# Kernel optimization log

Hardware: AMD Instinct MI355X
Metric: run time of the kernel (lower is better)

The kernel has to match this reference:

```python
import jax, jax.numpy as jnp
import numpy as np

EPS = 1e-12  # torch F.normalize clamp

N, C, H, W = 32, 128, 128, 128
K = 64  # num_clusters


def setup_inputs() -> dict:
    key = jax.random.key(0)
    k1, k2, k3 = jax.random.split(key, 3)
    x = jax.random.normal(k1, (N, C, H, W), dtype=jnp.float32)
    conv_w = jax.random.normal(k2, (K, C), dtype=jnp.float32) * 0.1  # 1x1 conv weight, no bias
    centroids = jax.random.uniform(k3, (K, C), dtype=jnp.float32)   # torch.rand init
    return {"x": x, "conv_w": conv_w, "centroids": centroids}


def reference(x, conv_w, centroids):
    n, c = x.shape[:2]
    xf = x.reshape(n, c, -1)                       # [N, C, S], S = H*W
    # 1x1 conv == per-location matmul over channels
    soft_assign = jnp.einsum('kc,ncs->nks', conv_w, xf)
    soft_assign = jax.nn.softmax(soft_assign, axis=1)   # softmax over clusters
    # vlad[n,k,c] = sum_s a[n,k,s] * (x[n,c,s] - centroid[k,c])
    #            = (a @ x^T) - (sum_s a) * centroid   (avoids per-cluster residual tensors)
    vlad = jnp.einsum('nks,ncs->nkc', soft_assign, xf) \
           - soft_assign.sum(axis=-1)[..., None] * centroids[None, :, :]
    # intra-normalization over descriptor dim
    vlad = vlad / jnp.maximum(jnp.linalg.norm(vlad, axis=2, keepdims=True), EPS)
    flat = vlad.reshape(n, -1)                     # [N, K*C]
    flat = flat / jnp.maximum(jnp.linalg.norm(flat, axis=1, keepdims=True), EPS)
    return flat
```

## Files before the change

kernel.cpp:

```cpp
#include <hip/hip_runtime.h>
#include <hip/hip_bf16.h>

#define N_ 32
#define C_ 128
#define K_ 64
#define S_ 16384
#define TS 32
#define NCHUNK 32
#define CHUNK (S_/NCHUNK)
#define NITER (CHUNK/TS)
#define CP 136
#define LP 68
#define SP 40
#define EPS 1e-12f

typedef __attribute__((ext_vector_type(8))) short short8;
typedef __attribute__((ext_vector_type(4))) float floatx4;

__device__ inline unsigned short bfraw(float v) {
  return __builtin_bit_cast(unsigned short, __float2bfloat16(v));
}
__device__ inline float bff(unsigned short u) {
  union { unsigned int i; float f; } c; c.i = ((unsigned int)u) << 16; return c.f;
}

template <bool SLAB>
__global__ __launch_bounds__(256, 4) void vlad_main(
    const float* __restrict__ x, const float* __restrict__ w,
    float* __restrict__ vlad_out, float* __restrict__ asum_out) {
  __shared__ unsigned short sXTh[TS * CP];
  __shared__ unsigned short sXTl[TS * CP];
  __shared__ float sLog[TS * LP];
  __shared__ unsigned short sPh[K_ * SP];

  const int tid = threadIdx.x;
  const int lane = tid & 63;
  const int wv = tid >> 6;
  const int n = blockIdx.x >> 5;
  const int chunk = blockIdx.x & 31;
  const int sbase = chunk * CHUNK;

  const int lm = lane & 15;
  const int lq = lane >> 4;
  const int kb = lq * 8;

  short8 Wh[4], Wl[4];
  {
    const float* wp = w + (wv * 16 + lm) * C_;
#pragma unroll
    for (int ks = 0; ks < 4; ++ks) {
      const float* p = wp + ks * 32 + kb;
      float4 a = *(const float4*)p;
      float4 b = *(const float4*)(p + 4);
      float e[8] = {a.x, a.y, a.z, a.w, b.x, b.y, b.z, b.w};
#pragma unroll
      for (int j = 0; j < 8; ++j) {
        unsigned short h = bfraw(e[j]);
        Wh[ks][j] = (short)h;
        Wl[ks][j] = (short)bfraw(e[j] - bff(h));
      }
    }
  }

  floatx4 acc[2][4];
#pragma unroll
  for (int i = 0; i < 2; ++i)
#pragma unroll
    for (int j = 0; j < 4; ++j) acc[i][j] = (floatx4){0.f, 0.f, 0.f, 0.f};
  float accA[8];
#pragma unroll
  for (int i = 0; i < 8; ++i) accA[i] = 0.f;

  const int cA = tid & 127, hA = tid >> 7;
  const float* xstg = x + ((size_t)n * C_ + cA) * S_ + sbase + hA * 16;
  const int sC = tid >> 3, octC = tid & 7;

  float4 p0 = *(const float4*)(xstg + 0);
  float4 p1 = *(const float4*)(xstg + 4);
  float4 p2 = *(const float4*)(xstg + 8);
  float4 p3 = *(const float4*)(xstg + 12);

  for (int t = 0; t < NITER; ++t) {
    const int s0 = sbase + t * TS;

    {
      float vv[16] = {p0.x,p0.y,p0.z,p0.w, p1.x,p1.y,p1.z,p1.w,
                      p2.x,p2.y,p2.z,p2.w, p3.x,p3.y,p3.z,p3.w};
      const int sb = hA * 16;
#pragma unroll
      for (int u = 0; u < 16; ++u) {
        unsigned short h = bfraw(vv[u]);
        sXTh[(sb + u) * CP + cA] = h;
        sXTl[(sb + u) * CP + cA] = bfraw(vv[u] - bff(h));
      }
    }
    if (t + 1 < NITER) {
      const float* p = xstg + (t + 1) * TS;
      p0 = *(const float4*)(p + 0);
      p1 = *(const float4*)(p + 4);
      p2 = *(const float4*)(p + 8);
      p3 = *(const float4*)(p + 12);
    }
    __syncthreads();

#pragma unroll
    for (int st = 0; st < 2; ++st) {
      floatx4 D = {0.f, 0.f, 0.f, 0.f};
      const int srow = st * 16 + lm;
#pragma unroll
      for (int ks = 0; ks < 4; ++ks) {
        short8 Ah = *(const short8*)&sXTh[srow * CP + ks * 32 + kb];
        short8 Al = *(const short8*)&sXTl[srow * CP + ks * 32 + kb];
        D = __builtin_amdgcn_mfma_f32_16x16x32_bf16(Ah, Wh[ks], D, 0, 0, 0);
        D = __builtin_amdgcn_mfma_f32_16x16x32_bf16(Al, Wh[ks], D, 0, 0, 0);
        D = __builtin_amdgcn_mfma_f32_16x16x32_bf16(Ah, Wl[ks], D, 0, 0, 0);
      }
      const int sD = st * 16 + lq * 4;
      const int kcD = wv * 16 + lm;
#pragma unroll
      for (int r = 0; r < 4; ++r) sLog[(sD + r) * LP + kcD] = D[r];
    }
    __syncthreads();

    short8 Ah2[2], Al2[2];
    {
      float4 xa[2], xb[2];
#pragma unroll
      for (int ci = 0; ci < 2; ++ci) {
        const int crow = (wv * 2 + ci) * 16 + lm;
        const float* xp = x + ((size_t)n * C_ + crow) * S_ + s0 + kb;
        xa[ci] = *(const float4*)xp;
        xb[ci] = *(const float4*)(xp + 4);
      }

      float e[8];
      float m = -1e30f;
#pragma unroll
      for (int i = 0; i < 8; ++i) {
        e[i] = sLog[sC * LP + octC + 8 * i];
        m = fmaxf(m, e[i]);
      }
      m = fmaxf(m, __shfl_xor(m, 1));
      m = fmaxf(m, __shfl_xor(m, 2));
      m = fmaxf(m, __shfl_xor(m, 4));
      float sum = 0.f;
#pragma unroll
      for (int i = 0; i < 8; ++i) { e[i] = __expf(e[i] - m); sum += e[i]; }
      sum += __shfl_xor(sum, 1);
      sum += __shfl_xor(sum, 2);
      sum += __shfl_xor(sum, 4);
      float inv = 1.f / sum;
#pragma unroll
      for (int i = 0; i < 8; ++i) {
        float pr = e[i] * inv;
        accA[i] += pr;
        sPh[(octC + 8 * i) * SP + sC] = bfraw(pr);
      }

#pragma unroll
      for (int ci = 0; ci < 2; ++ci) {
        float ee[8] = {xa[ci].x, xa[ci].y, xa[ci].z, xa[ci].w,
                       xb[ci].x, xb[ci].y, xb[ci].z, xb[ci].w};
#pragma unroll
        for (int j = 0; j < 8; ++j) {
          unsigned short h = bfraw(ee[j]);
          Ah2[ci][j] = (short)h;
          Al2[ci][j] = (short)bfraw(ee[j] - bff(h));
        }
      }
    }
    __syncthreads();

    {
      short8 Bh[4];
#pragma unroll
      for (int kt = 0; kt < 4; ++kt)
        Bh[kt] = *(const short8*)&sPh[(kt * 16 + lm) * SP + kb];
#pragma unroll
      for (int ci = 0; ci < 2; ++ci) {
#pragma unroll
        for (int kt = 0; kt < 4; ++kt) {
          acc[ci][kt] = __builtin_amdgcn_mfma_f32_16x16x32_bf16(Ah2[ci], Bh[kt], acc[ci][kt], 0, 0, 0);
          acc[ci][kt] = __builtin_amdgcn_mfma_f32_16x16x32_bf16(Al2[ci], Bh[kt], acc[ci][kt], 0, 0, 0);
        }
      }
    }
    __syncthreads();
  }

  float* vb = vlad_out + (SLAB ? (size_t)blockIdx.x : (size_t)n) * (K_ * C_);
#pragma unroll
  for (int ci = 0; ci < 2; ++ci) {
    const int c0 = (wv * 2 + ci) * 16 + lq * 4;
#pragma unroll
    for (int kt = 0; kt < 4; ++kt) {
      const int kc = kt * 16 + lm;
      if (SLAB) {
        *(floatx4*)(vb + kc * C_ + c0) = acc[ci][kt];
      } else {
#pragma unroll
        for (int r = 0; r < 4; ++r)
          atomicAdd(vb + kc * C_ + c0 + r, acc[ci][kt][r]);
      }
    }
  }

#pragma unroll
  for (int i = 0; i < 8; ++i) sLog[tid * 8 + i] = accA[i];
  __syncthreads();
  if (tid < K_) {
    float tsum = 0.f;
    for (int s8 = 0; s8 < 32; ++s8)
      tsum += sLog[(s8 * 8 + (tid & 7)) * 8 + (tid >> 3)];
    if (SLAB) asum_out[(size_t)blockIdx.x * K_ + tid] = tsum;
    else atomicAdd(asum_out + n * K_ + tid, tsum);
  }
}

template <bool SLAB>
__global__ __launch_bounds__(128) void vlad_intra(
    const float* __restrict__ vlad_in, const float* __restrict__ asum_in,
    const float* __restrict__ cent, float* __restrict__ vlad_norm,
    float* __restrict__ gnorm) {
  const int bid = blockIdx.x;
  const int n = bid >> 6, k = bid & 63;
  const int c = threadIdx.x;

  float v, a;
  if (SLAB) {
    v = 0.f; a = 0.f;
#pragma unroll 4
    for (int ch = 0; ch < NCHUNK; ++ch) {
      v += vlad_in[((size_t)(n * NCHUNK + ch) * K_ + k) * C_ + c];
      a += asum_in[(n * NCHUNK + ch) * K_ + k];
    }
  } else {
    v = vlad_in[((size_t)(n * K_ + k)) * C_ + c];
    a = asum_in[n * K_ + k];
  }
  v -= a * cent[k * C_ + c];

  float ss = v * v;
  ss += __shfl_xor(ss, 1);  ss += __shfl_xor(ss, 2);  ss += __shfl_xor(ss, 4);
  ss += __shfl_xor(ss, 8);  ss += __shfl_xor(ss, 16); ss += __shfl_xor(ss, 32);
  __shared__ float red[2];
  if ((threadIdx.x & 63) == 0) red[threadIdx.x >> 6] = ss;
  __syncthreads();
  float total = red[0] + red[1];
  float nrm = fmaxf(sqrtf(total), EPS);
  vlad_norm[((size_t)(n * K_ + k)) * C_ + c] = v / nrm;
  if (threadIdx.x == 0) atomicAdd(gnorm + n, total / (nrm * nrm));
}

__global__ __launch_bounds__(256) void vlad_final(
    const float* __restrict__ vlad_norm, const float* __restrict__ gnorm,
    float* __restrict__ out) {
  const int idx = blockIdx.x * 256 + threadIdx.x;
  if (idx >= N_ * K_ * C_) return;
  float g = gnorm[idx >> 13];
  out[idx] = vlad_norm[idx] / fmaxf(sqrtf(g), EPS);
}

extern "C" void kernel_launch(void* const* d_in, const int* in_sizes, int n_in,
                              void* d_out, int out_size, void* d_ws, size_t ws_size,
                              hipStream_t stream) {
  const float* x    = (const float*)d_in[0];
  const float* w    = (const float*)d_in[1];
  const float* cent = (const float*)d_in[2];
  float* out = (float*)d_out;

  const int nblk = N_ * NCHUNK;
  const size_t slab_f  = (size_t)nblk * K_ * C_;
  const size_t asum_f  = (size_t)nblk * K_;
  const size_t norm_f  = (size_t)N_ * K_ * C_;
  const size_t need = (slab_f + asum_f + norm_f + N_) * sizeof(float);

  if (ws_size >= need) {
    float* slab   = (float*)d_ws;
    float* asums  = slab + slab_f;
    float* vnorm  = asums + asum_f;
    float* gnorm  = vnorm + norm_f;
    hipMemsetAsync(gnorm, 0, N_ * sizeof(float), stream);
    vlad_main<true><<<dim3(nblk), dim3(256), 0, stream>>>(x, w, slab, asums);
    vlad_intra<true><<<dim3(N_ * K_), dim3(128), 0, stream>>>(slab, asums, cent, vnorm, gnorm);
    vlad_final<<<dim3((N_ * K_ * C_ + 255) / 256), dim3(256), 0, stream>>>(vnorm, gnorm, out);
  } else {
    float* vlad_acc = (float*)d_ws;
    float* asum_g   = vlad_acc + norm_f;
    float* gnorm    = asum_g + N_ * K_;
    hipMemsetAsync(d_ws, 0, (norm_f + N_ * K_ + N_) * sizeof(float), stream);
    vlad_main<false><<<dim3(nblk), dim3(256), 0, stream>>>(x, w, vlad_acc, asum_g);
    vlad_intra<false><<<dim3(N_ * K_), dim3(128), 0, stream>>>(vlad_acc, asum_g, cent, vlad_acc, gnorm);
    vlad_final<<<dim3((N_ * K_ * C_ + 255) / 256), dim3(256), 0, stream>>>(vlad_acc, gnorm, out);
  }
}
```

Baseline: 442.6 us.

## Rewrite main VLAD kernel with single-pass fp16 MFMA and register softmax

```diff
diff --git a/kernel.cpp b/kernel.cpp
--- a/kernel.cpp
+++ b/kernel.cpp
@@ -1,197 +1,188 @@
 #include <hip/hip_runtime.h>
-#include <hip/hip_bf16.h>
 
 #define N_ 32
 #define C_ 128
 #define K_ 64
 #define S_ 16384
-#define TS 32
-#define NCHUNK 32
-#define CHUNK (S_/NCHUNK)
-#define NITER (CHUNK/TS)
-#define CP 136
-#define LP 68
-#define SP 40
+#define TS 64
+#define NBPN 24
+#define NTILES (S_/TS)
+#define NBLK (N_*NBPN)
+#define XS 136
+#define WS 136
+#define PS 72
 #define EPS 1e-12f
 
-typedef __attribute__((ext_vector_type(8))) short short8;
+typedef __attribute__((ext_vector_type(8))) _Float16 half8;
+typedef __attribute__((ext_vector_type(4))) _Float16 half4;
 typedef __attribute__((ext_vector_type(4))) float floatx4;
 
-__device__ inline unsigned short bfraw(float v) {
-  return __builtin_bit_cast(unsigned short, __float2bfloat16(v));
-}
-__device__ inline float bff(unsigned short u) {
-  union { unsigned int i; float f; } c; c.i = ((unsigned int)u) << 16; return c.f;
+__device__ __forceinline__ int swz(int row, int c) {
+  return (((c >> 4) ^ (row & 7)) << 4) | (c & 15);
 }
 
 template <bool SLAB>
 __global__ __launch_bounds__(256, 4) void vlad_main(
     const float* __restrict__ x, const float* __restrict__ w,
     float* __restrict__ vlad_out, float* __restrict__ asum_out) {
-  __shared__ unsigned short sXTh[TS * CP];
-  __shared__ unsigned short sXTl[TS * CP];
-  __shared__ float sLog[TS * LP];
-  __shared__ unsigned short sPh[K_ * SP];
+  __shared__ _Float16 sXT[TS * XS];
+  __shared__ _Float16 sW[K_ * WS];
+  __shared__ _Float16 sP[K_ * PS];
+  __shared__ float sRed[4 * K_];
 
   const int tid = threadIdx.x;
   const int lane = tid & 63;
   const int wv = tid >> 6;
-  const int n = blockIdx.x >> 5;
-  const int chunk = blockIdx.x & 31;
-  const int sbase = chunk * CHUNK;
-
   const int lm = lane & 15;
-  const int lq = lane >> 4;
-  const int kb = lq * 8;
-
-  short8 Wh[4], Wl[4];
+  const int quad = lane >> 4;
+
+  const int bid = blockIdx.x;
+  const int n = bid / NBPN;
+  const int j = bid % NBPN;
+  const int ts = (j * NTILES) / NBPN;
+  const int te = ((j + 1) * NTILES) / NBPN;
+
+  for (int idx = tid; idx < K_ * C_; idx += 256) {
+    int kc = idx >> 7, c = idx & 127;
+    sW[kc * WS + swz(kc, c)] = (_Float16)w[idx];
+  }
+
+  floatx4 acc[2][4];
+#pragma unroll
+  for (int i = 0; i < 2; ++i)
+#pragma unroll
+    for (int k = 0; k < 4; ++k) acc[i][k] = (floatx4){0.f, 0.f, 0.f, 0.f};
+  float accA[4] = {0.f, 0.f, 0.f, 0.f};
+
+  const int cw = tid & 15;
+  const int sq = tid >> 4;
+  const float* xn = x + (size_t)n * C_ * S_;
+
+  float4 pf[8];
   {
-    const float* wp = w + (wv * 16 + lm) * C_;
+    const float* p = xn + (size_t)(8 * cw) * S_ + ts * TS + 4 * sq;
+#pragma unroll
+    for (int r = 0; r < 8; ++r) pf[r] = *(const float4*)(p + (size_t)r * S_);
+  }
+
+  __syncthreads();
+
+  for (int t = ts; t < te; ++t) {
+    const int s0 = t * TS;
+
+#pragma unroll
+    for (int u = 0; u < 4; ++u) {
+      const int s = 4 * sq + u;
+      half8 hv;
+#pragma unroll
+      for (int r = 0; r < 8; ++r) {
+        float f = (u == 0) ? pf[r].x : (u == 1) ? pf[r].y : (u == 2) ? pf[r].z : pf[r].w;
+        hv[r] = (_Float16)f;
+      }
+      *(half8*)&sXT[s * XS + swz(s, 8 * cw)] = hv;
+    }
+    __syncthreads();
+
+    float4 gxa[2][2];
+#pragma unroll
+    for (int ci = 0; ci < 2; ++ci) {
+      const float* p = xn + (size_t)((2 * wv + ci) * 16 + lm) * S_ + s0 + quad * 8;
+      gxa[ci][0] = *(const float4*)p;
+      gxa[ci][1] = *(const float4*)(p + 4);
+    }
+
+    floatx4 D[4];
+#pragma unroll
+    for (int k = 0; k < 4; ++k) D[k] = (floatx4){0.f, 0.f, 0.f, 0.f};
+    const int srow = wv * 16 + lm;
 #pragma unroll
     for (int ks = 0; ks < 4; ++ks) {
-      const float* p = wp + ks * 32 + kb;
-      float4 a = *(const float4*)p;
-      float4 b = *(const float4*)(p + 4);
-      float e[8] = {a.x, a.y, a.z, a.w, b.x, b.y, b.z, b.w};
-#pragma unroll
-      for (int j = 0; j < 8; ++j) {
-        unsigned short h = bfraw(e[j]);
-        Wh[ks][j] = (short)h;
-        Wl[ks][j] = (short)bfraw(e[j] - bff(h));
-      }
-    }
-  }
-
-  floatx4 acc[2][4];
-#pragma unroll
-  for (int i = 0; i < 2; ++i)
-#pragma unroll
-    for (int j = 0; j < 4; ++j) acc[i][j] = (floatx4){0.f, 0.f, 0.f, 0.f};
-  float accA[8];
-#pragma unroll
-  for (int i = 0; i < 8; ++i) accA[i] = 0.f;
-
-  const int cA = tid & 127, hA = tid >> 7;
-  const float* xstg = x + ((size_t)n * C_ + cA) * S_ + sbase + hA * 16;
-  const int sC = tid >> 3, octC = tid & 7;
-
-  float4 p0 = *(const float4*)(xstg + 0);
-  float4 p1 = *(const float4*)(xstg + 4);
-  float4 p2 = *(const float4*)(xstg + 8);
-  float4 p3 = *(const float4*)(xstg + 12);
-
-  for (int t = 0; t < NITER; ++t) {
-    const int s0 = sbase + t * TS;
-
-    {
-      float vv[16] = {p0.x,p0.y,p0.z,p0.w, p1.x,p1.y,p1.z,p1.w,
-                      p2.x,p2.y,p2.z,p2.w, p3.x,p3.y,p3.z,p3.w};
-      const int sb = hA * 16;
-#pragma unroll
-      for (int u = 0; u < 16; ++u) {
-        unsigned short h = bfraw(vv[u]);
-        sXTh[(sb + u) * CP + cA] = h;
-        sXTl[(sb + u) * CP + cA] = bfraw(vv[u] - bff(h));
-      }
-    }
-    if (t + 1 < NITER) {
-      const float* p = xstg + (t + 1) * TS;
-      p0 = *(const float4*)(p + 0);
-      p1 = *(const float4*)(p + 4);
-      p2 = *(const float4*)(p + 8);
-      p3 = *(const float4*)(p + 12);
-    }
-    __syncthreads();
-
-#pragma unroll
-    for (int st = 0; st < 2; ++st) {
-      floatx4 D = {0.f, 0.f, 0.f, 0.f};
-      const int srow = st * 16 + lm;
-#pragma unroll
-      for (int ks = 0; ks < 4; ++ks) {
-        short8 Ah = *(const short8*)&sXTh[srow * CP + ks * 32 + kb];
-        short8 Al = *(const short8*)&sXTl[srow * CP + ks * 32 + kb];
-        D = __builtin_amdgcn_mfma_f32_16x16x32_bf16(Ah, Wh[ks], D, 0, 0, 0);
-        D = __builtin_amdgcn_mfma_f32_16x16x32_bf16(Al, Wh[ks], D, 0, 0, 0);
-        D = __builtin_amdgcn_mfma_f32_16x16x32_bf16(Ah, Wl[ks], D, 0, 0, 0);
-      }
-      const int sD = st * 16 + lq * 4;
-      const int kcD = wv * 16 + lm;
-#pragma unroll
-      for (int r = 0; r < 4; ++r) sLog[(sD + r) * LP + kcD] = D[r];
-    }
-    __syncthreads();
-
-    short8 Ah2[2], Al2[2];
-    {
-      float4 xa[2], xb[2];
-#pragma unroll
-      for (int ci = 0; ci < 2; ++ci) {
-        const int crow = (wv * 2 + ci) * 16 + lm;
-        const float* xp = x + ((size_t)n * C_ + crow) * S_ + s0 + kb;
-        xa[ci] = *(const float4*)xp;
-        xb[ci] = *(const float4*)(xp + 4);
-      }
-
-      float e[8];
-      float m = -1e30f;
-#pragma unroll
-      for (int i = 0; i < 8; ++i) {
-        e[i] = sLog[sC * LP + octC + 8 * i];
-        m = fmaxf(m, e[i]);
-      }
+      half8 Af = *(const half8*)&sXT[srow * XS + swz(srow, ks * 32 + quad * 8)];
+#pragma unroll
+      for (int kt = 0; kt < 4; ++kt) {
+        const int krow = kt * 16 + lm;
+        half8 Wf = *(const half8*)&sW[krow * WS + swz(krow, ks * 32 + quad * 8)];
+        D[kt] = __builtin_amdgcn_mfma_f32_16x16x32_f16(Af, Wf, D[kt], 0, 0, 0);
+      }
+    }
+
+#pragma unroll
+    for (int r = 0; r < 4; ++r) {
+      float m = fmaxf(fmaxf(D[0][r], D[1][r]), fmaxf(D[2][r], D[3][r]));
       m = fmaxf(m, __shfl_xor(m, 1));
       m = fmaxf(m, __shfl_xor(m, 2));
       m = fmaxf(m, __shfl_xor(m, 4));
-      float sum = 0.f;
-#pragma unroll
-      for (int i = 0; i < 8; ++i) { e[i] = __expf(e[i] - m); sum += e[i]; }
+      m = fmaxf(m, __shfl_xor(m, 8));
+      float e0 = __expf(D[0][r] - m), e1 = __expf(D[1][r] - m),
+            e2 = __expf(D[2][r] - m), e3 = __expf(D[3][r] - m);
+      float sum = e0 + e1 + e2 + e3;
       sum += __shfl_xor(sum, 1);
       sum += __shfl_xor(sum, 2);
       sum += __shfl_xor(sum, 4);
+      sum += __shfl_xor(sum, 8);
       float inv = 1.f / sum;
-#pragma unroll
-      for (int i = 0; i < 8; ++i) {
-        float pr = e[i] * inv;
-        accA[i] += pr;
-        sPh[(octC + 8 * i) * SP + sC] = bfraw(pr);
-      }
-
+      D[0][r] = e0 * inv; D[1][r] = e1 * inv;
+      D[2][r] = e2 * inv; D[3][r] = e3 * inv;
+    }
+#pragma unroll
+    for (int kt = 0; kt < 4; ++kt) {
+      accA[kt] += D[kt][0] + D[kt][1] + D[kt][2] + D[kt][3];
+      half4 hp = {(_Float16)D[kt][0], (_Float16)D[kt][1],
+                  (_Float16)D[kt][2], (_Float16)D[kt][3]};
+      *(half4*)&sP[(kt * 16 + lm) * PS + wv * 16 + quad * 4] = hp;
+    }
+    float4 gxb[2][2];
+#pragma unroll
+    for (int ci = 0; ci < 2; ++ci) {
+      const float* p = xn + (size_t)((2 * wv + ci) * 16 + lm) * S_ + s0 + 32 + quad * 8;
+      gxb[ci][0] = *(const float4*)p;
+      gxb[ci][1] = *(const float4*)(p + 4);
+    }
+    __syncthreads();
+
+    {
+      half8 Bp[4];
+#pragma unroll
+      for (int kt = 0; kt < 4; ++kt)
+        Bp[kt] = *(const half8*)&sP[(kt * 16 + lm) * PS + quad * 8];
 #pragma unroll
       for (int ci = 0; ci < 2; ++ci) {
-        float ee[8] = {xa[ci].x, xa[ci].y, xa[ci].z, xa[ci].w,
-                       xb[ci].x, xb[ci].y, xb[ci].z, xb[ci].w};
-#pragma unroll
-        for (int j = 0; j < 8; ++j) {
-          unsigned short h = bfraw(ee[j]);
-          Ah2[ci][j] = (short)h;
-          Al2[ci][j] = (short)bfraw(ee[j] - bff(h));
-        }
-      }
-    }
-    __syncthreads();
-
+        half8 Ax = {(_Float16)gxa[ci][0].x, (_Float16)gxa[ci][0].y,
+                    (_Float16)gxa[ci][0].z, (_Float16)gxa[ci][0].w,
+                    (_Float16)gxa[ci][1].x, (_Float16)gxa[ci][1].y,
+                    (_Float16)gxa[ci][1].z, (_Float16)gxa[ci][1].w};
+#pragma unroll
+        for (int kt = 0; kt < 4; ++kt)
+          acc[ci][kt] = __builtin_amdgcn_mfma_f32_16x16x32_f16(Ax, Bp[kt], acc[ci][kt], 0, 0, 0);
+      }
+    }
+    if (t + 1 < te) {
+      const float* p = xn + (size_t)(8 * cw) * S_ + (t + 1) * TS + 4 * sq;
+#pragma unroll
+      for (int r = 0; r < 8; ++r) pf[r] = *(const float4*)(p + (size_t)r * S_);
+    }
     {
-      short8 Bh[4];
+      half8 Bp[4];
 #pragma unroll
       for (int kt = 0; kt < 4; ++kt)
-        Bh[kt] = *(const short8*)&sPh[(kt * 16 + lm) * SP + kb];
+        Bp[kt] = *(const half8*)&sP[(kt * 16 + lm) * PS + 32 + quad * 8];
 #pragma unroll
       for (int ci = 0; ci < 2; ++ci) {
-#pragma unroll
-        for (int kt = 0; kt < 4; ++kt) {
-          acc[ci][kt] = __builtin_amdgcn_mfma_f32_16x16x32_bf16(Ah2[ci], Bh[kt], acc[ci][kt], 0, 0, 0);
-          acc[ci][kt] = __builtin_amdgcn_mfma_f32_16x16x32_bf16(Al2[ci], Bh[kt], acc[ci][kt], 0, 0, 0);
-        }
-      }
-    }
-    __syncthreads();
-  }
-
-  float* vb = vlad_out + (SLAB ? (size_t)blockIdx.x : (size_t)n) * (K_ * C_);
+        half8 Ax = {(_Float16)gxb[ci][0].x, (_Float16)gxb[ci][0].y,
+                    (_Float16)gxb[ci][0].z, (_Float16)gxb[ci][0].w,
+                    (_Float16)gxb[ci][1].x, (_Float16)gxb[ci][1].y,
+                    (_Float16)gxb[ci][1].z, (_Float16)gxb[ci][1].w};
+#pragma unroll
+        for (int kt = 0; kt < 4; ++kt)
+          acc[ci][kt] = __builtin_amdgcn_mfma_f32_16x16x32_f16(Ax, Bp[kt], acc[ci][kt], 0, 0, 0);
+      }
+    }
+  }
+
+  float* vb = vlad_out + (SLAB ? (size_t)bid : (size_t)n) * (K_ * C_);
 #pragma unroll
   for (int ci = 0; ci < 2; ++ci) {
-    const int c0 = (wv * 2 + ci) * 16 + lq * 4;
+    const int c0 = (2 * wv + ci) * 16 + quad * 4;
 #pragma unroll
     for (int kt = 0; kt < 4; ++kt) {
       const int kc = kt * 16 + lm;
@@ -206,14 +197,17 @@
   }
 
 #pragma unroll
-  for (int i = 0; i < 8; ++i) sLog[tid * 8 + i] = accA[i];
+  for (int kt = 0; kt < 4; ++kt) {
+    float v = accA[kt];
+    v += __shfl_xor(v, 16);
+    v += __shfl_xor(v, 32);
+    if (quad == 0) sRed[wv * K_ + kt * 16 + lm] = v;
+  }
   __syncthreads();
   if (tid < K_) {
-    float tsum = 0.f;
-    for (int s8 = 0; s8 < 32; ++s8)
-      tsum += sLog[(s8 * 8 + (tid & 7)) * 8 + (tid >> 3)];
-    if (SLAB) asum_out[(size_t)blockIdx.x * K_ + tid] = tsum;
-    else atomicAdd(asum_out + n * K_ + tid, tsum);
+    float s = sRed[tid] + sRed[K_ + tid] + sRed[2 * K_ + tid] + sRed[3 * K_ + tid];
+    if (SLAB) asum_out[(size_t)bid * K_ + tid] = s;
+    else atomicAdd(asum_out + n * K_ + tid, s);
   }
 }
 
@@ -230,9 +224,9 @@
   if (SLAB) {
     v = 0.f; a = 0.f;
 #pragma unroll 4
-    for (int ch = 0; ch < NCHUNK; ++ch) {
-      v += vlad_in[((size_t)(n * NCHUNK + ch) * K_ + k) * C_ + c];
-      a += asum_in[(n * NCHUNK + ch) * K_ + k];
+    for (int ch = 0; ch < NBPN; ++ch) {
+      v += vlad_in[((size_t)(n * NBPN + ch) * K_ + k) * C_ + c];
+      a += asum_in[(n * NBPN + ch) * K_ + k];
     }
   } else {
     v = vlad_in[((size_t)(n * K_ + k)) * C_ + c];
@@ -269,19 +263,18 @@
   const float* cent = (const float*)d_in[2];
   float* out = (float*)d_out;
 
-  const int nblk = N_ * NCHUNK;
-  const size_t slab_f  = (size_t)nblk * K_ * C_;
-  const size_t asum_f  = (size_t)nblk * K_;
-  const size_t norm_f  = (size_t)N_ * K_ * C_;
+  const size_t slab_f = (size_t)NBLK * K_ * C_;
+  const size_t asum_f = (size_t)NBLK * K_;
+  const size_t norm_f = (size_t)N_ * K_ * C_;
   const size_t need = (slab_f + asum_f + norm_f + N_) * sizeof(float);
 
   if (ws_size >= need) {
-    float* slab   = (float*)d_ws;
-    float* asums  = slab + slab_f;
-    float* vnorm  = asums + asum_f;
-    float* gnorm  = vnorm + norm_f;
+    float* slab  = (float*)d_ws;
+    float* asums = slab + slab_f;
+    float* vnorm = asums + asum_f;
+    float* gnorm = vnorm + norm_f;
     hipMemsetAsync(gnorm, 0, N_ * sizeof(float), stream);
-    vlad_main<true><<<dim3(nblk), dim3(256), 0, stream>>>(x, w, slab, asums);
+    vlad_main<true><<<dim3(NBLK), dim3(256), 0, stream>>>(x, w, slab, asums);
     vlad_intra<true><<<dim3(N_ * K_), dim3(128), 0, stream>>>(slab, asums, cent, vnorm, gnorm);
     vlad_final<<<dim3((N_ * K_ * C_ + 255) / 256), dim3(256), 0, stream>>>(vnorm, gnorm, out);
   } else {
@@ -289,7 +282,7 @@
     float* asum_g   = vlad_acc + norm_f;
     float* gnorm    = asum_g + N_ * K_;
     hipMemsetAsync(d_ws, 0, (norm_f + N_ * K_ + N_) * sizeof(float), stream);
-    vlad_main<false><<<dim3(nblk), dim3(256), 0, stream>>>(x, w, vlad_acc, asum_g);
+    vlad_main<false><<<dim3(NBLK), dim3(256), 0, stream>>>(x, w, vlad_acc, asum_g);
     vlad_intra<false><<<dim3(N_ * K_), dim3(128), 0, stream>>>(vlad_acc, asum_g, cent, vlad_acc, gnorm);
     vlad_final<<<dim3((N_ * K_ * C_ + 255) / 256), dim3(256), 0, stream>>>(vlad_acc, gnorm, out);
   }
```

New measurement: 414.8 us. 1.07x faster.
